# Kernel tuning notes

Measured on AMD Instinct MI355X. Metric: run time of the kernel, lower is better.

## Reference

```python
import jax, jax.numpy as jnp
import numpy as np

B, N, D = 32, 1024, 3
Z_SCALES = jnp.array([2.0, 4.0, 8.0, 16.0, 32.0], dtype=jnp.float32)
Z_DIM = 16.0
BETA = 0.01          # kl_warmup done (epoch >= kl_warmup_epochs), so beta == args.beta
SINK_EPS = 0.1       # entropic regularization for the EMD (Sinkhorn) approximation
SINK_ITERS = 20
BIG = 1e8
NEG = -1e9


def _sqdist(x, y):
    # x: [B,N,D], y: [B,M,D] -> squared euclidean distances [B,N,M]
    xx = jnp.sum(x * x, -1)[:, :, None]
    yy = jnp.sum(y * y, -1)[:, None, :]
    xy = jnp.einsum('bnd,bmd->bnm', x, y)
    return jnp.maximum(xx + yy - 2.0 * xy, 0.0)


def _chamfer(x, xm, y, ym):
    # masked bidirectional chamfer: mean over valid points, mean over batch
    d = _sqdist(x, y)                                             # [B,N,M]
    d_xy = jnp.min(jnp.where(ym[:, None, :], d, BIG), axis=2)     # [B,N]
    d_yx = jnp.min(jnp.where(xm[:, :, None], d, BIG), axis=1)     # [B,M]
    nx = jnp.sum(xm, -1).astype(x.dtype)
    ny = jnp.sum(ym, -1).astype(x.dtype)
    cd = (jnp.sum(jnp.where(xm, d_xy, 0.0), -1) / nx
          + jnp.sum(jnp.where(ym, d_yx, 0.0), -1) / ny)
    return jnp.mean(cd)


def _emd_sinkhorn(x, xm, y, ym):
    # entropic-OT approximation of the masked EMD (log-domain Sinkhorn)
    C = _sqdist(x, y)                                             # [B,N,M]
    C = jnp.where(xm[:, :, None] & ym[:, None, :], C, BIG)
    nx = jnp.sum(xm, -1).astype(x.dtype)                          # [B]
    ny = jnp.sum(ym, -1).astype(x.dtype)
    log_a = jnp.where(xm, -jnp.log(nx)[:, None], NEG)             # [B,N]
    log_b = jnp.where(ym, -jnp.log(ny)[:, None], NEG)             # [B,M]

    @jax.checkpoint
    def step(carry, _):
        f, g = carry
        f = SINK_EPS * (log_a - jax.nn.logsumexp((g[:, None, :] - C) / SINK_EPS, axis=2))
        g = SINK_EPS * (log_b - jax.nn.logsumexp((f[:, :, None] - C) / SINK_EPS, axis=1))
        return (f, g), None

    f0 = jnp.zeros_like(log_a)
    g0 = jnp.zeros_like(log_b)
    (f, g), _ = jax.lax.scan(step, (f0, g0), None, length=SINK_ITERS)
    logP = (f[:, :, None] + g[:, None, :] - C) / SINK_EPS         # transport plan (log)
    emd = jnp.sum(jnp.exp(logP) * C, axis=(1, 2))                 # [B]
    return jnp.mean(emd)


def setup_inputs() -> dict:
    key = jax.random.key(0)
    k1, k2, k3 = jax.random.split(key, 3)
    return {
        'output_set': jax.random.normal(k1, (B, N, D), dtype=jnp.float32),
        'output_mask': jnp.ones((B, N), dtype=bool),
        'target_set': jax.random.normal(k2, (B, N, D), dtype=jnp.float32),
        'target_mask': jnp.ones((B, N), dtype=bool),
        'kls': jax.random.uniform(k3, (B, Z_SCALES.shape[0]), dtype=jnp.float32),
    }


def reference(output_set, output_mask, target_set, target_mask, kls):
    cd = _chamfer(output_set, output_mask, target_set, target_mask)
    emd = _emd_sinkhorn(output_set, output_mask, target_set, target_mask)
    recon_loss = cd + emd
    kl_loss = jnp.mean(jnp.sum(kls, axis=1))
    loss = BETA * kl_loss + recon_loss
    topdown_kl = jnp.mean(kls, axis=0) / (Z_SCALES * Z_DIM)        # [L]
    return loss, kl_loss, recon_loss, topdown_kl
```

## Files before the change

kernel.cpp:

```cpp
#include <hip/hip_runtime.h>
#include <math.h>

#define BB 32
#define NN 1024
#define NEGV (-1e9f)
#define BIGC (1e8f)
#define EPSS 0.1f
#define K2f   14.426950408889634f
#define TWOK2 28.853900817779268f
#define INVK2 0.06931471805599453f
#define SINK_ITERS 20
#define CHUNKS 16
#define NBLK (BB * CHUNKS)
#define BARSTRIDE 32

typedef float f32x2 __attribute__((ext_vector_type(2)));

__device__ __forceinline__ float wave_reduce_sum(float v) {
#pragma unroll
  for (int s = 32; s >= 1; s >>= 1) v += __shfl_xor(v, s, 64);
  return v;
}
__device__ __forceinline__ float wave_reduce_max(float v) {
#pragma unroll
  for (int s = 32; s >= 1; s >>= 1) v = fmaxf(v, __shfl_xor(v, s, 64));
  return v;
}
__device__ __forceinline__ float wave_reduce_min(float v) {
#pragma unroll
  for (int s = 32; s >= 1; s >>= 1) v = fminf(v, __shfl_xor(v, s, 64));
  return v;
}

__device__ __forceinline__ bool getbit(const unsigned* mb, int i) {
  return (mb[i >> 5] >> (i & 31)) & 1u;
}

__device__ __forceinline__ void pot_st2(float* p, float lo, float hi) {
  const unsigned long long pk =
      ((unsigned long long)__float_as_uint(hi) << 32) | __float_as_uint(lo);
  __hip_atomic_store((unsigned long long*)p, pk, __ATOMIC_RELAXED,
                     __HIP_MEMORY_SCOPE_AGENT);
}
__device__ __forceinline__ void pot_ld2(const float* p, float& lo, float& hi) {
  const unsigned long long pk = __hip_atomic_load(
      (const unsigned long long*)p, __ATOMIC_RELAXED, __HIP_MEMORY_SCOPE_AGENT);
  lo = __uint_as_float((unsigned)pk);
  hi = __uint_as_float((unsigned)(pk >> 32));
}
__device__ __forceinline__ float pot_ld(const float* p) {
  return __hip_atomic_load(p, __ATOMIC_RELAXED, __HIP_MEMORY_SCOPE_AGENT);
}

__device__ __forceinline__ void batch_barrier(int* bp, int gen, int tid) {
  __syncthreads();
  if (tid == 0) {
    __hip_atomic_fetch_add(bp, 1, __ATOMIC_RELAXED, __HIP_MEMORY_SCOPE_AGENT);
    const int target = CHUNKS * gen;
    while (__hip_atomic_load(bp, __ATOMIC_RELAXED, __HIP_MEMORY_SCOPE_AGENT) < target)
      __builtin_amdgcn_s_sleep(2);
    (void)__hip_atomic_load(bp, __ATOMIC_ACQUIRE, __HIP_MEMORY_SCOPE_WORKGROUP);
  }
  __syncthreads();
}

template<bool CHAMF>
__device__ __forceinline__ void twopass(
    const float4* rl, const float4* cl, const float* Agl, const unsigned* rmb,
    float elab, int c, int wave, int lane, int tid,
    float* __restrict__ potOut, size_t base,
    float invnb, int b, float* __restrict__ cdPart, float* reds)
{
  float cdacc = 0.0f;
#pragma unroll 1
  for (int grp = 0; grp < 2; ++grp) {
    const int row0 = c * 64 + wave * 8 + grp * 4;

    float xs0[4], xs1[4], xs2[4], xw[4];
    bool rmv[4];
#pragma unroll
    for (int r = 0; r < 4; ++r) {
      const float4 xp = rl[row0 + r];
      xs0[r] = TWOK2 * xp.x; xs1[r] = TWOK2 * xp.y; xs2[r] = TWOK2 * xp.z;
      xw[r] = xp.w;
      rmv[r] = getbit(rmb, row0 + r);
    }

    float u[4][16];
#pragma unroll
    for (int j = 0; j < 16; ++j) {
      const int m = lane + j * 64;
      const float4 yp = cl[m];
      const float aj = Agl[m];
#pragma unroll
      for (int r = 0; r < 4; ++r) {
        float t = fmaf(xs0[r], yp.x, aj);
        t = fmaf(xs1[r], yp.y, t);
        t = fmaf(xs2[r], yp.z, t);
        u[r][j] = t;
      }
    }

    float gm[4];
#pragma unroll
    for (int r = 0; r < 4; ++r) {
      const float a0 = fmaxf(fmaxf(u[r][0], u[r][1]), u[r][2]);
      const float a1 = fmaxf(fmaxf(u[r][3], u[r][4]), u[r][5]);
      const float a2 = fmaxf(fmaxf(u[r][6], u[r][7]), u[r][8]);
      const float a3 = fmaxf(fmaxf(u[r][9], u[r][10]), u[r][11]);
      const float a4 = fmaxf(fmaxf(u[r][12], u[r][13]), u[r][14]);
      const float mr = fmaxf(fmaxf(fmaxf(a0, a1), a2),
                             fmaxf(fmaxf(a3, a4), u[r][15]));
      gm[r] = wave_reduce_max(mr);
    }

    float ss[4] = {0.f, 0.f, 0.f, 0.f};
#pragma unroll
    for (int j = 0; j < 16; ++j) {
#pragma unroll
      for (int r = 0; r < 4; ++r)
        ss[r] += __builtin_amdgcn_exp2f(u[r][j] - gm[r]);
    }
#pragma unroll
    for (int r = 0; r < 4; ++r) ss[r] = wave_reduce_sum(ss[r]);

    float pv[4];
#pragma unroll
    for (int r = 0; r < 4; ++r) {
      const float lse2 = gm[r] + __builtin_amdgcn_logf(ss[r]);
      const float el = rmv[r] ? elab : (EPSS * NEGV);
      pv[r] = el + xw[r] - INVK2 * lse2;
    }
    if (lane == 0) {
      pot_st2(&potOut[base + row0 + 0], pv[0], pv[1]);
      pot_st2(&potOut[base + row0 + 2], pv[2], pv[3]);
      if constexpr (CHAMF) {
#pragma unroll
        for (int r = 0; r < 4; ++r)
          if (rmv[r]) cdacc += fmaxf(fmaf(-INVK2, gm[r], xw[r]), 0.0f);
      }
    }
  }

  if constexpr (CHAMF) {
    if (lane == 0) reds[wave] = cdacc;
    __syncthreads();
    if (tid == 0) {
      float s = 0.f;
#pragma unroll
      for (int w = 0; w < 8; ++w) s += reds[w];
      cdPart[(size_t)b * CHUNKS + c] = s * invnb * (1.0f / BB);
    }
  }
}

__device__ __forceinline__ void onepass(
    const float4* rl, const float4* cl, const float* Agl, const unsigned* rmb,
    float elab, int row0, int lane, float* __restrict__ pot, size_t base,
    float fp[8])
{
  f32x2 xs0[4], xs1[4], xs2[4], sh2[4], acc2[4];
  bool rmv[8];
#pragma unroll
  for (int p = 0; p < 4; ++p) {
    const float4 xa = rl[row0 + 2 * p];
    const float4 xb = rl[row0 + 2 * p + 1];
    rmv[2 * p]     = getbit(rmb, row0 + 2 * p);
    rmv[2 * p + 1] = getbit(rmb, row0 + 2 * p + 1);
    xs0[p] = f32x2{TWOK2 * xa.x, TWOK2 * xb.x};
    xs1[p] = f32x2{TWOK2 * xa.y, TWOK2 * xb.y};
    xs2[p] = f32x2{TWOK2 * xa.z, TWOK2 * xb.z};
    sh2[p] = f32x2{
        rmv[2 * p]     ? (K2f * (elab + xa.w - fp[2 * p]))     : 3.0e38f,
        rmv[2 * p + 1] ? (K2f * (elab + xb.w - fp[2 * p + 1])) : 3.0e38f};
    acc2[p] = f32x2{0.f, 0.f};
  }

#pragma unroll 4
  for (int j = 0; j < 16; ++j) {
    const int m = lane + j * 64;
    const float4 q = cl[m];
    const float aj = Agl[m];
    const f32x2 qx = {q.x, q.x}, qy = {q.y, q.y}, qz = {q.z, q.z};
    const f32x2 aj2 = {aj, aj};
#pragma unroll
    for (int p = 0; p < 4; ++p) {
      f32x2 t = __builtin_elementwise_fma(xs0[p], qx, aj2);
      t = __builtin_elementwise_fma(xs1[p], qy, t);
      t = __builtin_elementwise_fma(xs2[p], qz, t);
      const f32x2 e = t - sh2[p];
      const f32x2 ex = {__builtin_amdgcn_exp2f(e.x), __builtin_amdgcn_exp2f(e.y)};
      acc2[p] += ex;
    }
  }

  float acc[8];
#pragma unroll
  for (int p = 0; p < 4; ++p) { acc[2 * p] = acc2[p].x; acc[2 * p + 1] = acc2[p].y; }
#pragma unroll
  for (int r = 0; r < 8; ++r) acc[r] = wave_reduce_sum(acc[r]);

#pragma unroll
  for (int r = 0; r < 8; ++r) {
    const float l2 = fminf(fmaxf(__builtin_amdgcn_logf(acc[r]), -120.0f), 120.0f);
    fp[r] = rmv[r] ? (fp[r] - INVK2 * l2) : (EPSS * NEGV);
  }
  if (lane == 0) {
#pragma unroll
    for (int r = 0; r < 8; r += 2)
      pot_st2(&pot[base + row0 + r], fp[r], fp[r + 1]);
  }
}

__global__ __launch_bounds__(512, 4) void fused_sink(
    const float* __restrict__ xset, const int* __restrict__ xm,
    const float* __restrict__ yset, const int* __restrict__ ym,
    float* __restrict__ f, float* __restrict__ g,
    float* __restrict__ cd_part, float* __restrict__ emd_part,
    int* __restrict__ bar)
{
  const int gid = blockIdx.x;
  const int b = gid & (BB - 1), c = gid >> 5;
  const int tid = threadIdx.x, wave = tid >> 6, lane = tid & 63;
  const size_t base = (size_t)b * NN;
  int* bp = bar + b * BARSTRIDE;

  __shared__ float4 xl[NN];
  __shared__ float4 yl[NN];
  __shared__ float Ag[NN];
  __shared__ float gvs[NN];
  __shared__ unsigned xmb[NN / 32], ymb[NN / 32];
  __shared__ float cred[16];
  __shared__ float reds[8];
  __shared__ float sscal[4];

  float cntx = 0.f, cnty = 0.f;
  for (int i = tid; i < NN; i += 512) {
    const size_t ix = (base + (size_t)i) * 3;
    const float x0 = xset[ix], x1 = xset[ix + 1], x2 = xset[ix + 2];
    const float y0 = yset[ix], y1 = yset[ix + 1], y2 = yset[ix + 2];
    xl[i] = make_float4(x0, x1, x2, x0 * x0 + x1 * x1 + x2 * x2);
    yl[i] = make_float4(y0, y1, y2, y0 * y0 + y1 * y1 + y2 * y2);
    const int mxv = xm[base + i], myv = ym[base + i];
    cntx += mxv ? 1.0f : 0.0f;
    cnty += myv ? 1.0f : 0.0f;
    const unsigned long long bx = __ballot(mxv != 0);
    const unsigned long long by = __ballot(myv != 0);
    if (lane == 0) {
      const int w0 = i >> 5;
      xmb[w0] = (unsigned)bx; xmb[w0 + 1] = (unsigned)(bx >> 32);
      ymb[w0] = (unsigned)by; ymb[w0 + 1] = (unsigned)(by >> 32);
    }
  }
  cntx = wave_reduce_sum(cntx);
  cnty = wave_reduce_sum(cnty);
  if (lane == 0) { cred[wave] = cntx; cred[8 + wave] = cnty; }
  __syncthreads();
  if (tid == 0) {
    float a = 0.f, cc = 0.f;
#pragma unroll
    for (int i = 0; i < 8; ++i) { a += cred[i]; cc += cred[8 + i]; }
    sscal[0] = -EPSS * logf(a);
    sscal[1] = -EPSS * logf(cc);
    sscal[2] = 1.0f / a;
    sscal[3] = 1.0f / cc;
  }
  __syncthreads();
  const float elax = sscal[0], elay = sscal[1], invx = sscal[2], invy = sscal[3];
  int gen = 0;

  for (int i = tid; i < NN; i += 512)
    Ag[i] = getbit(ymb, i) ? (-K2f * yl[i].w) : -1e30f;
  __syncthreads();
  twopass<true>(xl, yl, Ag, xmb, elax, c, wave, lane, tid, f, base,
                invx, b, cd_part, reds);

  for (int i = tid; i < NN; i += 512)
    gvs[i] = getbit(xmb, i) ? xl[i].w : BIGC;
  __syncthreads();
  {
    float acc = 0.0f;
#pragma unroll 1
    for (int rr = 0; rr < 8; ++rr) {
      const int row = c * 64 + wave * 8 + rr;
      const float4 yp = yl[row];
      const float ys0 = -2.f * yp.x, ys1 = -2.f * yp.y, ys2 = -2.f * yp.z;
      float dmin = BIGC;
#pragma unroll
      for (int j = 0; j < 16; ++j) {
        const int m = lane + j * 64;
        const float4 xq = xl[m];
        float d = fmaf(ys0, xq.x, gvs[m]);
        d = fmaf(ys1, xq.y, d);
        d = fmaf(ys2, xq.z, d);
        dmin = fminf(dmin, d);
      }
      dmin = wave_reduce_min(dmin);
      if (lane == 0 && getbit(ymb, row)) acc += fmaxf(yp.w + dmin, 0.0f);
    }
    __syncthreads();
    if (lane == 0) reds[wave] = acc;
    __syncthreads();
    if (tid == 0) {
      float s = 0.f;
#pragma unroll
      for (int w = 0; w < 8; ++w) s += reds[w];
      cd_part[BB * CHUNKS + (size_t)b * CHUNKS + c] = s * invy * (1.0f / BB);
    }
  }

  batch_barrier(bp, ++gen, tid);

  {
    const int i2 = tid << 1;
    float f0, f1;
    pot_ld2(&f[base + i2], f0, f1);
    Ag[i2]     = getbit(xmb, i2)     ? fmaf(K2f, f0, -K2f * xl[i2].w)     : -1e30f;
    Ag[i2 + 1] = getbit(xmb, i2 + 1) ? fmaf(K2f, f1, -K2f * xl[i2 + 1].w) : -1e30f;
  }
  __syncthreads();
  twopass<false>(yl, xl, Ag, ymb, elay, c, wave, lane, tid, g, base,
                 0.f, b, nullptr, reds);

  float myf[8], myg[8];
  __syncthreads();
  {
    const int row0w = c * 64 + wave * 8;
#pragma unroll
    for (int r = 0; r < 8; r += 2) {
      pot_ld2(&f[base + row0w + r], myf[r], myf[r + 1]);
      pot_ld2(&g[base + row0w + r], myg[r], myg[r + 1]);
    }
  }

  batch_barrier(bp, ++gen, tid);

  const int row0w = c * 64 + wave * 8;
  for (int it = 1; it < SINK_ITERS; ++it) {
    {
      const int i2 = tid << 1;
      float g0, g1;
      pot_ld2(&g[base + i2], g0, g1);
      Ag[i2]     = getbit(ymb, i2)     ? fmaf(K2f, g0, -K2f * yl[i2].w)     : -1e30f;
      Ag[i2 + 1] = getbit(ymb, i2 + 1) ? fmaf(K2f, g1, -K2f * yl[i2 + 1].w) : -1e30f;
    }
    __syncthreads();
    onepass(xl, yl, Ag, xmb, elax, row0w, lane, f, base, myf);
    batch_barrier(bp, ++gen, tid);

    {
      const int i2 = tid << 1;
      float f0, f1;
      pot_ld2(&f[base + i2], f0, f1);
      Ag[i2]     = getbit(xmb, i2)     ? fmaf(K2f, f0, -K2f * xl[i2].w)     : -1e30f;
      Ag[i2 + 1] = getbit(xmb, i2 + 1) ? fmaf(K2f, f1, -K2f * xl[i2 + 1].w) : -1e30f;
    }
    __syncthreads();
    onepass(yl, xl, Ag, ymb, elay, row0w, lane, g, base, myg);
    batch_barrier(bp, ++gen, tid);
  }

  {
    const int i2 = tid << 1;
    float g0, g1;
    pot_ld2(&g[base + i2], g0, g1);
    gvs[i2] = g0; gvs[i2 + 1] = g1;
    Ag[i2]     = getbit(ymb, i2)     ? fmaf(K2f, g0, -K2f * yl[i2].w)     : -1e30f;
    Ag[i2 + 1] = getbit(ymb, i2 + 1) ? fmaf(K2f, g1, -K2f * yl[i2 + 1].w) : -1e30f;
  }
  __syncthreads();
  {
    float acc = 0.0f;
#pragma unroll 1
    for (int rr = 0; rr < 8; ++rr) {
      const int row = c * 64 + wave * 8 + rr;
      const float4 xp = xl[row];
      const float fv = pot_ld(&f[base + row]);
      const float rc = fmaf(K2f, fv, -K2f * xp.w);
      const float xs0 = TWOK2 * xp.x, xs1 = TWOK2 * xp.y, xs2 = TWOK2 * xp.z;
      const bool rv = getbit(xmb, row);
#pragma unroll
      for (int j = 0; j < 16; ++j) {
        const int m = lane + j * 64;
        const float4 yp = yl[m];
        const float a = rv ? (Ag[m] + rc) : -1e30f;
        float t = fmaf(xs0, yp.x, a);
        t = fmaf(xs1, yp.y, t);
        t = fmaf(xs2, yp.z, t);
        float C = fmaf(t, -INVK2, fv + gvs[m]);
        C = fmaxf(C, 0.0f);
        acc = fmaf(__builtin_amdgcn_exp2f(t), C, acc);
      }
    }
    acc = wave_reduce_sum(acc);
    __syncthreads();
    if (lane == 0) reds[wave] = acc;
    __syncthreads();
    if (tid == 0) {
      float s = 0.f;
#pragma unroll
      for (int w = 0; w < 8; ++w) s += reds[w];
      emd_part[(size_t)b * CHUNKS + c] = s * (1.0f / BB);
    }
  }
}

__global__ __launch_bounds__(1024) void prep_kernel(
    const float* __restrict__ xset, const int* __restrict__ xm,
    const float* __restrict__ yset, const int* __restrict__ ym,
    float4* __restrict__ xpack, float4* __restrict__ ypack,
    float* __restrict__ elax, float* __restrict__ elay,
    float* __restrict__ invx, float* __restrict__ invy)
{
  const int b = blockIdx.x;
  const int n = threadIdx.x;
  const size_t idx = (size_t)b * NN + n;

  const float x0 = xset[idx * 3 + 0], x1 = xset[idx * 3 + 1], x2 = xset[idx * 3 + 2];
  const float y0 = yset[idx * 3 + 0], y1 = yset[idx * 3 + 1], y2 = yset[idx * 3 + 2];
  xpack[idx] = make_float4(x0, x1, x2, x0 * x0 + x1 * x1 + x2 * x2);
  ypack[idx] = make_float4(y0, y1, y2, y0 * y0 + y1 * y1 + y2 * y2);

  float cx = wave_reduce_sum(xm[idx] ? 1.0f : 0.0f);
  float cy = wave_reduce_sum(ym[idx] ? 1.0f : 0.0f);

  __shared__ float sx[16], sy[16];
  const int wave = n >> 6, lane = n & 63;
  if (lane == 0) { sx[wave] = cx; sy[wave] = cy; }
  __syncthreads();
  if (n == 0) {
    float a = 0.0f, c = 0.0f;
#pragma unroll
    for (int i = 0; i < 16; ++i) { a += sx[i]; c += sy[i]; }
    elax[b] = -EPSS * logf(a);
    elay[b] = -EPSS * logf(c);
    invx[b] = 1.0f / a;
    invy[b] = 1.0f / c;
  }
}

template<bool FIRST, bool CHAMF>
__global__ __launch_bounds__(512) void sink_step(
    const float4* __restrict__ rowpk, const float4* __restrict__ redpk,
    const int* __restrict__ rowmask, const int* __restrict__ redmask,
    const float* __restrict__ pot_in, float* __restrict__ pot_out,
    const float* __restrict__ ela,
    const float* __restrict__ invn,
    float* __restrict__ cd_part)
{
  const int b = blockIdx.y, chunk = blockIdx.x, tid = threadIdx.x;
  const int wave = tid >> 6, lane = tid & 63;
  const size_t base = (size_t)b * NN;

  __shared__ float4 ypk[NN];
  __shared__ float Aj[NN];
  __shared__ float reds[8];

  for (int i = tid; i < NN; i += 512) {
    const float4 yp = redpk[base + i];
    ypk[i] = yp;
    float a;
    if constexpr (FIRST)
      a = redmask[base + i] ? (-K2f * yp.w) : -1e30f;
    else
      a = redmask[base + i] ? fmaf(K2f, pot_in[base + i], -K2f * yp.w) : -1e30f;
    Aj[i] = a;
  }
  __syncthreads();

  const float elab = ela[b];
  float cdacc = 0.0f;

#pragma unroll 1
  for (int grp = 0; grp < 2; ++grp) {
    const int row0 = chunk * 64 + wave * 8 + grp * 4;

    float xs0[4], xs1[4], xs2[4], xw[4];
    int rmv[4];
#pragma unroll
    for (int r = 0; r < 4; ++r) {
      const float4 xp = rowpk[base + row0 + r];
      xs0[r] = TWOK2 * xp.x; xs1[r] = TWOK2 * xp.y; xs2[r] = TWOK2 * xp.z;
      xw[r] = xp.w;
      rmv[r] = rowmask[base + row0 + r];
    }

    float u[4][16];
#pragma unroll
    for (int j = 0; j < 16; ++j) {
      const int m = lane + j * 64;
      const float4 yp = ypk[m];
      const float aj = Aj[m];
#pragma unroll
      for (int r = 0; r < 4; ++r) {
        float t = fmaf(xs0[r], yp.x, aj);
        t = fmaf(xs1[r], yp.y, t);
        t = fmaf(xs2[r], yp.z, t);
        u[r][j] = t;
      }
    }

    float gm[4];
#pragma unroll
    for (int r = 0; r < 4; ++r) {
      const float a0 = fmaxf(fmaxf(u[r][0], u[r][1]), u[r][2]);
      const float a1 = fmaxf(fmaxf(u[r][3], u[r][4]), u[r][5]);
      const float a2 = fmaxf(fmaxf(u[r][6], u[r][7]), u[r][8]);
      const float a3 = fmaxf(fmaxf(u[r][9], u[r][10]), u[r][11]);
      const float a4 = fmaxf(fmaxf(u[r][12], u[r][13]), u[r][14]);
      const float mr = fmaxf(fmaxf(fmaxf(a0, a1), a2),
                             fmaxf(fmaxf(a3, a4), u[r][15]));
      gm[r] = wave_reduce_max(mr);
    }

    float ss[4] = {0.f, 0.f, 0.f, 0.f};
#pragma unroll
    for (int j = 0; j < 16; ++j) {
#pragma unroll
      for (int r = 0; r < 4; ++r)
        ss[r] += __builtin_amdgcn_exp2f(u[r][j] - gm[r]);
    }
#pragma unroll
    for (int r = 0; r < 4; ++r) ss[r] = wave_reduce_sum(ss[r]);

    if (lane == 0) {
#pragma unroll
      for (int r = 0; r < 4; ++r) {
        const float lse2 = gm[r] + __builtin_amdgcn_logf(ss[r]);
        const float el = rmv[r] ? elab : (EPSS * NEGV);
        pot_out[base + row0 + r] = el + xw[r] - INVK2 * lse2;
        if constexpr (CHAMF) {
          if (rmv[r])
            cdacc += fmaxf(fmaf(-INVK2, gm[r], xw[r]), 0.0f);
        }
      }
    }
  }

  if constexpr (CHAMF) {
    if (lane == 0) reds[wave] = cdacc;
    __syncthreads();
    if (tid == 0) {
      float s = 0.f;
#pragma unroll
      for (int w = 0; w < 8; ++w) s += reds[w];
      cd_part[(size_t)b * CHUNKS + chunk] = s * invn[b] * (1.0f / BB);
    }
  }
}

__global__ __launch_bounds__(512) void sink_fast(
    const float4* __restrict__ rowpk, const float4* __restrict__ redpk,
    const int* __restrict__ rowmask, const int* __restrict__ redmask,
    const float* __restrict__ pot_in, float* __restrict__ fpot,
    const float* __restrict__ ela)
{
  const int b = blockIdx.y, chunk = blockIdx.x, tid = threadIdx.x;
  const int wave = tid >> 6, lane = tid & 63;
  const size_t base = (size_t)b * NN;

  __shared__ float4 colq[NN];

  for (int i = tid; i < NN; i += 512) {
    const float4 yp = redpk[base + i];
    const float aj = redmask[base + i]
        ? fmaf(K2f, pot_in[base + i], -K2f * yp.w) : -1e30f;
    colq[i] = make_float4(yp.x, yp.y, yp.z, aj);
  }
  __syncthreads();

  const float elab = ela[b];
  const int row0 = chunk * 64 + wave * 8;

  float xs0[8], xs1[8], xs2[8], sh[8], acc[8], fp[8];
  int rmv[8];
#pragma unroll
  for (int r = 0; r < 8; ++r) {
    const float4 xp = rowpk[base + row0 + r];
    rmv[r] = rowmask[base + row0 + r];
    fp[r] = fpot[base + row0 + r];
    xs0[r] = TWOK2 * xp.x; xs1[r] = TWOK2 * xp.y; xs2[r] = TWOK2 * xp.z;
    sh[r] = rmv[r] ? (K2f * (elab + xp.w - fp[r])) : 3.0e38f;
    acc[r] = 0.0f;
  }

#pragma unroll 4
  for (int j = 0; j < 16; ++j) {
    const float4 q = colq[lane + j * 64];
#pragma unroll
    for (int r = 0; r < 8; ++r) {
      float t = fmaf(xs0[r], q.x, q.w);
      t = fmaf(xs1[r], q.y, t);
      t = fmaf(xs2[r], q.z, t);
      acc[r] += __builtin_amdgcn_exp2f(t - sh[r]);
    }
  }

#pragma unroll
  for (int r = 0; r < 8; ++r) acc[r] = wave_reduce_sum(acc[r]);

  if (lane == 0) {
#pragma unroll
    for (int r = 0; r < 8; ++r) {
      const float l2 = fminf(fmaxf(__builtin_amdgcn_logf(acc[r]), -120.0f), 120.0f);
      fpot[base + row0 + r] = rmv[r] ? (fp[r] - INVK2 * l2) : (EPSS * NEGV);
    }
  }
}

__global__ __launch_bounds__(512) void chamfer_dir(
    const float4* __restrict__ rowpk, const float4* __restrict__ redpk,
    const int* __restrict__ rowmask, const int* __restrict__ redmask,
    const float* __restrict__ invn, float* __restrict__ part)
{
  const int b = blockIdx.y, chunk = blockIdx.x, tid = threadIdx.x;
  const int wave = tid >> 6, lane = tid & 63;
  const size_t base = (size_t)b * NN;

  __shared__ float4 xw4[NN];
  for (int i = tid; i < NN; i += 512) {
    float4 xp = redpk[base + i];
    xp.w = redmask[base + i] ? xp.w : BIGC;
    xw4[i] = xp;
  }
  __syncthreads();

  float acc = 0.0f;
#pragma unroll 1
  for (int rr = 0; rr < 8; ++rr) {
    const int row = chunk * 64 + wave * 8 + rr;
    const float4 yp = rowpk[base + row];
    const float ys0 = -2.f * yp.x, ys1 = -2.f * yp.y, ys2 = -2.f * yp.z;
    float dmin = BIGC;
#pragma unroll
    for (int j = 0; j < 16; ++j) {
      const float4 xq = xw4[lane + j * 64];
      float d = fmaf(ys0, xq.x, xq.w);
      d = fmaf(ys1, xq.y, d);
      d = fmaf(ys2, xq.z, d);
      dmin = fminf(dmin, d);
    }
    dmin = wave_reduce_min(dmin);
    if (lane == 0 && rowmask[base + row]) acc += fmaxf(yp.w + dmin, 0.0f);
  }

  __shared__ float reds[8];
  if (lane == 0) reds[wave] = acc;
  __syncthreads();
  if (tid == 0) {
    float s = 0.f;
#pragma unroll
    for (int w = 0; w < 8; ++w) s += reds[w];
    part[(size_t)b * CHUNKS + chunk] = s * invn[b] * (1.0f / BB);
  }
}

__global__ __launch_bounds__(512) void emd_kernel(
    const float4* __restrict__ rowpk, const float4* __restrict__ redpk,
    const int* __restrict__ rowmask, const int* __restrict__ redmask,
    const float* __restrict__ frow, const float* __restrict__ gred,
    float* __restrict__ part)
{
  const int b = blockIdx.y, chunk = blockIdx.x, tid = threadIdx.x;
  const int wave = tid >> 6, lane = tid & 63;
  const size_t base = (size_t)b * NN;

  __shared__ float4 ypk[NN];
  __shared__ float Ag[NN];
  __shared__ float gv[NN];
  for (int i = tid; i < NN; i += 512) {
    const float4 yp = redpk[base + i];
    ypk[i] = yp;
    const float gg = gred[base + i];
    gv[i] = gg;
    Ag[i] = redmask[base + i] ? fmaf(K2f, gg, -K2f * yp.w) : -1e30f;
  }
  __syncthreads();

  float acc = 0.0f;
#pragma unroll 1
  for (int rr = 0; rr < 8; ++rr) {
    const int row = chunk * 64 + wave * 8 + rr;
    const float4 xp = rowpk[base + row];
    const float fv = frow[base + row];
    const float rc = fmaf(K2f, fv, -K2f * xp.w);
    const float xs0 = TWOK2 * xp.x, xs1 = TWOK2 * xp.y, xs2 = TWOK2 * xp.z;
    const bool rv = rowmask[base + row] != 0;
#pragma unroll
    for (int j = 0; j < 16; ++j) {
      const int m = lane + j * 64;
      const float4 yp = ypk[m];
      const float a = rv ? (Ag[m] + rc) : -1e30f;
      float t = fmaf(xs0, yp.x, a);
      t = fmaf(xs1, yp.y, t);
      t = fmaf(xs2, yp.z, t);
      float C = fmaf(t, -INVK2, fv + gv[m]);
      C = fmaxf(C, 0.0f);
      acc = fmaf(__builtin_amdgcn_exp2f(t), C, acc);
    }
  }

  acc = wave_reduce_sum(acc);
  __shared__ float reds[8];
  if (lane == 0) reds[wave] = acc;
  __syncthreads();
  if (tid == 0) {
    float s = 0.f;
#pragma unroll
    for (int w = 0; w < 8; ++w) s += reds[w];
    part[(size_t)b * CHUNKS + chunk] = s * (1.0f / BB);
  }
}

__global__ __launch_bounds__(256) void final_kernel(
    const float* __restrict__ cd_part, const float* __restrict__ emd_part,
    const float* __restrict__ kls, float* __restrict__ out)
{
  const int tid = threadIdx.x, wave = tid >> 6, lane = tid & 63;
  __shared__ float sh[12];
  float s1 = 0.f, s2 = 0.f, s3 = 0.f;
  for (int i = tid; i < 2 * BB * CHUNKS; i += 256) s1 += cd_part[i];
  for (int i = tid; i < BB * CHUNKS; i += 256) s2 += emd_part[i];
  for (int i = tid; i < BB * 5; i += 256) s3 += kls[i];
  s1 = wave_reduce_sum(s1); s2 = wave_reduce_sum(s2); s3 = wave_reduce_sum(s3);
  if (lane == 0) { sh[wave] = s1; sh[4 + wave] = s2; sh[8 + wave] = s3; }
  __syncthreads();
  if (tid == 0) {
    const float cd = sh[0] + sh[1] + sh[2] + sh[3];
    const float emd = sh[4] + sh[5] + sh[6] + sh[7];
    const float kl = (sh[8] + sh[9] + sh[10] + sh[11]) / (float)BB;
    out[0] = 0.01f * kl + (cd + emd);
    out[1] = kl;
    out[2] = cd + emd;
  }
  if (tid < 5) {
    float cs = 0.f;
    for (int b2 = 0; b2 < BB; ++b2) cs += kls[b2 * 5 + tid];
    const float zs[5] = {2.f, 4.f, 8.f, 16.f, 32.f};
    out[3 + tid] = (cs / (float)BB) / (zs[tid] * 16.f);
  }
}

extern "C" void kernel_launch(void* const* d_in, const int* in_sizes, int n_in,
                              void* d_out, int out_size, void* d_ws, size_t ws_size,
                              hipStream_t stream)
{
  const float* xset = (const float*)d_in[0];
  const int*   xm   = (const int*)d_in[1];
  const float* yset = (const float*)d_in[2];
  const int*   ym   = (const int*)d_in[3];
  const float* kls  = (const float*)d_in[4];

  float* ws = (float*)d_ws;
  float*  f    = ws;
  float*  g    = f + BB * NN;
  float*  cd   = g + BB * NN;
  float*  emdp = cd + 2 * BB * CHUNKS;
  float*  elax = emdp + BB * CHUNKS;
  float*  elay = elax + BB;
  float*  invx = elay + BB;
  float*  invy = invx + BB;
  int*    bar  = (int*)(invy + BB);
  float4* xp4  = (float4*)(ws + 68256);
  float4* yp4  = xp4 + BB * NN;

  hipMemsetAsync(bar, 0, BB * BARSTRIDE * sizeof(int), stream);

  void* args[] = {(void*)&xset, (void*)&xm, (void*)&yset, (void*)&ym,
                  (void*)&f, (void*)&g, (void*)&cd, (void*)&emdp, (void*)&bar};
  hipError_t cerr = hipLaunchCooperativeKernel(
      reinterpret_cast<void*>(fused_sink), dim3(NBLK), dim3(512), args, 0, stream);

  if (cerr != hipSuccess) {
    prep_kernel<<<dim3(BB), 1024, 0, stream>>>(xset, xm, yset, ym,
                                               xp4, yp4, elax, elay, invx, invy);
    const dim3 sg(CHUNKS, BB);
    sink_step<true, true><<<sg, 512, 0, stream>>>(xp4, yp4, xm, ym, nullptr, f,
                                                  elax, invx, cd);
    chamfer_dir<<<sg, 512, 0, stream>>>(yp4, xp4, ym, xm, invy, cd + BB * CHUNKS);
    sink_step<false, false><<<sg, 512, 0, stream>>>(yp4, xp4, ym, xm, f, g,
                                                    elay, nullptr, nullptr);
    for (int it = 1; it < SINK_ITERS; ++it) {
      sink_fast<<<sg, 512, 0, stream>>>(xp4, yp4, xm, ym, g, f, elax);
      sink_fast<<<sg, 512, 0, stream>>>(yp4, xp4, ym, xm, f, g, elay);
    }
    emd_kernel<<<sg, 512, 0, stream>>>(xp4, yp4, xm, ym, f, g, emdp);
  }

  final_kernel<<<1, 256, 0, stream>>>(cd, emdp, kls, (float*)d_out);
}
```

Baseline: 382.9 us.

## Interleave two batch streams per block to hide inter-block barrier latency

After: 480.5 us. +25.5%, slower.

```diff
diff --git a/kernel.cpp b/kernel.cpp
--- a/kernel.cpp
+++ b/kernel.cpp
@@ -11,7 +11,7 @@
 #define INVK2 0.06931471805599453f
 #define SINK_ITERS 20
 #define CHUNKS 16
-#define NBLK (BB * CHUNKS)
+#define NBLK 256
 #define BARSTRIDE 32
 
 typedef float f32x2 __attribute__((ext_vector_type(2)));
@@ -52,13 +52,16 @@
   return __hip_atomic_load(p, __ATOMIC_RELAXED, __HIP_MEMORY_SCOPE_AGENT);
 }
 
-__device__ __forceinline__ void batch_barrier(int* bp, int gen, int tid) {
-  __syncthreads();
+__device__ __forceinline__ void bar_arrive(int* bp, int tid) {
+  __syncthreads();
+  if (tid == 0)
+    __hip_atomic_fetch_add(bp, 1, __ATOMIC_RELAXED, __HIP_MEMORY_SCOPE_AGENT);
+}
+__device__ __forceinline__ void bar_wait(int* bp, int gen, int tid) {
   if (tid == 0) {
-    __hip_atomic_fetch_add(bp, 1, __ATOMIC_RELAXED, __HIP_MEMORY_SCOPE_AGENT);
     const int target = CHUNKS * gen;
     while (__hip_atomic_load(bp, __ATOMIC_RELAXED, __HIP_MEMORY_SCOPE_AGENT) < target)
-      __builtin_amdgcn_s_sleep(2);
+      __builtin_amdgcn_s_sleep(1);
     (void)__hip_atomic_load(bp, __ATOMIC_ACQUIRE, __HIP_MEMORY_SCOPE_WORKGROUP);
   }
   __syncthreads();
@@ -212,28 +215,13 @@
   }
 }
 
-__global__ __launch_bounds__(512, 4) void fused_sink(
+__device__ __forceinline__ void stage_stream(
     const float* __restrict__ xset, const int* __restrict__ xm,
     const float* __restrict__ yset, const int* __restrict__ ym,
-    float* __restrict__ f, float* __restrict__ g,
-    float* __restrict__ cd_part, float* __restrict__ emd_part,
-    int* __restrict__ bar)
-{
-  const int gid = blockIdx.x;
-  const int b = gid & (BB - 1), c = gid >> 5;
-  const int tid = threadIdx.x, wave = tid >> 6, lane = tid & 63;
-  const size_t base = (size_t)b * NN;
-  int* bp = bar + b * BARSTRIDE;
-
-  __shared__ float4 xl[NN];
-  __shared__ float4 yl[NN];
-  __shared__ float Ag[NN];
-  __shared__ float gvs[NN];
-  __shared__ unsigned xmb[NN / 32], ymb[NN / 32];
-  __shared__ float cred[16];
-  __shared__ float reds[8];
-  __shared__ float sscal[4];
-
+    size_t base, int tid, int lane, int wave,
+    float4* xl, float4* yl, unsigned* xmb, unsigned* ymb,
+    float* cred, float* sscal4)
+{
   float cntx = 0.f, cnty = 0.f;
   for (int i = tid; i < NN; i += 512) {
     const size_t ix = (base + (size_t)i) * 3;
@@ -260,106 +248,88 @@
     float a = 0.f, cc = 0.f;
 #pragma unroll
     for (int i = 0; i < 8; ++i) { a += cred[i]; cc += cred[8 + i]; }
-    sscal[0] = -EPSS * logf(a);
-    sscal[1] = -EPSS * logf(cc);
-    sscal[2] = 1.0f / a;
-    sscal[3] = 1.0f / cc;
-  }
-  __syncthreads();
-  const float elax = sscal[0], elay = sscal[1], invx = sscal[2], invy = sscal[3];
-  int gen = 0;
-
+    sscal4[0] = -EPSS * logf(a);
+    sscal4[1] = -EPSS * logf(cc);
+    sscal4[2] = 1.0f / a;
+    sscal4[3] = 1.0f / cc;
+  }
+  __syncthreads();
+}
+
+__device__ __forceinline__ void build_ag_first(
+    const float4* yl, const unsigned* ymb, float* Ag, int tid)
+{
   for (int i = tid; i < NN; i += 512)
     Ag[i] = getbit(ymb, i) ? (-K2f * yl[i].w) : -1e30f;
   __syncthreads();
-  twopass<true>(xl, yl, Ag, xmb, elax, c, wave, lane, tid, f, base,
-                invx, b, cd_part, reds);
-
+}
+__device__ __forceinline__ void build_ag_pot(
+    const float4* pl, const unsigned* pmb, const float* pot, size_t base,
+    float* Ag, int tid)
+{
+  const int i2 = tid << 1;
+  float p0, p1;
+  pot_ld2(&pot[base + i2], p0, p1);
+  Ag[i2]     = getbit(pmb, i2)     ? fmaf(K2f, p0, -K2f * pl[i2].w)     : -1e30f;
+  Ag[i2 + 1] = getbit(pmb, i2 + 1) ? fmaf(K2f, p1, -K2f * pl[i2 + 1].w) : -1e30f;
+  __syncthreads();
+}
+
+__device__ __forceinline__ void chamfer_yx(
+    const float4* xl, const float4* yl, const unsigned* xmb, const unsigned* ymb,
+    float* gvs, float* reds, int c, int wave, int lane, int tid,
+    float invy, int b, float* __restrict__ cd_part)
+{
   for (int i = tid; i < NN; i += 512)
     gvs[i] = getbit(xmb, i) ? xl[i].w : BIGC;
   __syncthreads();
-  {
-    float acc = 0.0f;
+  float acc = 0.0f;
 #pragma unroll 1
-    for (int rr = 0; rr < 8; ++rr) {
-      const int row = c * 64 + wave * 8 + rr;
-      const float4 yp = yl[row];
-      const float ys0 = -2.f * yp.x, ys1 = -2.f * yp.y, ys2 = -2.f * yp.z;
-      float dmin = BIGC;
-#pragma unroll
-      for (int j = 0; j < 16; ++j) {
-        const int m = lane + j * 64;
-        const float4 xq = xl[m];
-        float d = fmaf(ys0, xq.x, gvs[m]);
-        d = fmaf(ys1, xq.y, d);
-        d = fmaf(ys2, xq.z, d);
-        dmin = fminf(dmin, d);
-      }
-      dmin = wave_reduce_min(dmin);
-      if (lane == 0 && getbit(ymb, row)) acc += fmaxf(yp.w + dmin, 0.0f);
-    }
-    __syncthreads();
-    if (lane == 0) reds[wave] = acc;
-    __syncthreads();
-    if (tid == 0) {
-      float s = 0.f;
-#pragma unroll
-      for (int w = 0; w < 8; ++w) s += reds[w];
-      cd_part[BB * CHUNKS + (size_t)b * CHUNKS + c] = s * invy * (1.0f / BB);
-    }
-  }
-
-  batch_barrier(bp, ++gen, tid);
-
-  {
-    const int i2 = tid << 1;
-    float f0, f1;
-    pot_ld2(&f[base + i2], f0, f1);
-    Ag[i2]     = getbit(xmb, i2)     ? fmaf(K2f, f0, -K2f * xl[i2].w)     : -1e30f;
-    Ag[i2 + 1] = getbit(xmb, i2 + 1) ? fmaf(K2f, f1, -K2f * xl[i2 + 1].w) : -1e30f;
-  }
-  __syncthreads();
-  twopass<false>(yl, xl, Ag, ymb, elay, c, wave, lane, tid, g, base,
-                 0.f, b, nullptr, reds);
-
-  float myf[8], myg[8];
-  __syncthreads();
-  {
-    const int row0w = c * 64 + wave * 8;
-#pragma unroll
-    for (int r = 0; r < 8; r += 2) {
-      pot_ld2(&f[base + row0w + r], myf[r], myf[r + 1]);
-      pot_ld2(&g[base + row0w + r], myg[r], myg[r + 1]);
-    }
-  }
-
-  batch_barrier(bp, ++gen, tid);
-
-  const int row0w = c * 64 + wave * 8;
-  for (int it = 1; it < SINK_ITERS; ++it) {
-    {
-      const int i2 = tid << 1;
-      float g0, g1;
-      pot_ld2(&g[base + i2], g0, g1);
-      Ag[i2]     = getbit(ymb, i2)     ? fmaf(K2f, g0, -K2f * yl[i2].w)     : -1e30f;
-      Ag[i2 + 1] = getbit(ymb, i2 + 1) ? fmaf(K2f, g1, -K2f * yl[i2 + 1].w) : -1e30f;
-    }
-    __syncthreads();
-    onepass(xl, yl, Ag, xmb, elax, row0w, lane, f, base, myf);
-    batch_barrier(bp, ++gen, tid);
-
-    {
-      const int i2 = tid << 1;
-      float f0, f1;
-      pot_ld2(&f[base + i2], f0, f1);
-      Ag[i2]     = getbit(xmb, i2)     ? fmaf(K2f, f0, -K2f * xl[i2].w)     : -1e30f;
-      Ag[i2 + 1] = getbit(xmb, i2 + 1) ? fmaf(K2f, f1, -K2f * xl[i2 + 1].w) : -1e30f;
-    }
-    __syncthreads();
-    onepass(yl, xl, Ag, ymb, elay, row0w, lane, g, base, myg);
-    batch_barrier(bp, ++gen, tid);
-  }
-
+  for (int rr = 0; rr < 8; ++rr) {
+    const int row = c * 64 + wave * 8 + rr;
+    const float4 yp = yl[row];
+    const float ys0 = -2.f * yp.x, ys1 = -2.f * yp.y, ys2 = -2.f * yp.z;
+    float dmin = BIGC;
+#pragma unroll
+    for (int j = 0; j < 16; ++j) {
+      const int m = lane + j * 64;
+      const float4 xq = xl[m];
+      float d = fmaf(ys0, xq.x, gvs[m]);
+      d = fmaf(ys1, xq.y, d);
+      d = fmaf(ys2, xq.z, d);
+      dmin = fminf(dmin, d);
+    }
+    dmin = wave_reduce_min(dmin);
+    if (lane == 0 && getbit(ymb, row)) acc += fmaxf(yp.w + dmin, 0.0f);
+  }
+  __syncthreads();
+  if (lane == 0) reds[wave] = acc;
+  __syncthreads();
+  if (tid == 0) {
+    float s = 0.f;
+#pragma unroll
+    for (int w = 0; w < 8; ++w) s += reds[w];
+    cd_part[BB * CHUNKS + (size_t)b * CHUNKS + c] = s * invy * (1.0f / BB);
+  }
+}
+
+__device__ __forceinline__ void pull_rows(
+    const float* f, const float* g, size_t base, int row0w,
+    float myf[8], float myg[8])
+{
+#pragma unroll
+  for (int r = 0; r < 8; r += 2) {
+    pot_ld2(&f[base + row0w + r], myf[r], myf[r + 1]);
+    pot_ld2(&g[base + row0w + r], myg[r], myg[r + 1]);
+  }
+}
+
+__device__ __forceinline__ void emd_eval(
+    const float4* xl, const float4* yl, const unsigned* xmb, const unsigned* ymb,
+    const float* f, const float* g, size_t base,
+    float* Ag, float* gvs, float* reds,
+    int c, int wave, int lane, int tid, int b, float* __restrict__ emd_part)
+{
   {
     const int i2 = tid << 1;
     float g0, g1;
@@ -369,40 +339,130 @@
     Ag[i2 + 1] = getbit(ymb, i2 + 1) ? fmaf(K2f, g1, -K2f * yl[i2 + 1].w) : -1e30f;
   }
   __syncthreads();
-  {
-    float acc = 0.0f;
+  float acc = 0.0f;
 #pragma unroll 1
-    for (int rr = 0; rr < 8; ++rr) {
-      const int row = c * 64 + wave * 8 + rr;
-      const float4 xp = xl[row];
-      const float fv = pot_ld(&f[base + row]);
-      const float rc = fmaf(K2f, fv, -K2f * xp.w);
-      const float xs0 = TWOK2 * xp.x, xs1 = TWOK2 * xp.y, xs2 = TWOK2 * xp.z;
-      const bool rv = getbit(xmb, row);
-#pragma unroll
-      for (int j = 0; j < 16; ++j) {
-        const int m = lane + j * 64;
-        const float4 yp = yl[m];
-        const float a = rv ? (Ag[m] + rc) : -1e30f;
-        float t = fmaf(xs0, yp.x, a);
-        t = fmaf(xs1, yp.y, t);
-        t = fmaf(xs2, yp.z, t);
-        float C = fmaf(t, -INVK2, fv + gvs[m]);
-        C = fmaxf(C, 0.0f);
-        acc = fmaf(__builtin_amdgcn_exp2f(t), C, acc);
-      }
-    }
-    acc = wave_reduce_sum(acc);
-    __syncthreads();
-    if (lane == 0) reds[wave] = acc;
-    __syncthreads();
-    if (tid == 0) {
-      float s = 0.f;
-#pragma unroll
-      for (int w = 0; w < 8; ++w) s += reds[w];
-      emd_part[(size_t)b * CHUNKS + c] = s * (1.0f / BB);
-    }
-  }
+  for (int rr = 0; rr < 8; ++rr) {
+    const int row = c * 64 + wave * 8 + rr;
+    const float4 xp = xl[row];
+    const float fv = pot_ld(&f[base + row]);
+    const float rc = fmaf(K2f, fv, -K2f * xp.w);
+    const float xs0 = TWOK2 * xp.x, xs1 = TWOK2 * xp.y, xs2 = TWOK2 * xp.z;
+    const bool rv = getbit(xmb, row);
+#pragma unroll
+    for (int j = 0; j < 16; ++j) {
+      const int m = lane + j * 64;
+      const float4 yp = yl[m];
+      const float a = rv ? (Ag[m] + rc) : -1e30f;
+      float t = fmaf(xs0, yp.x, a);
+      t = fmaf(xs1, yp.y, t);
+      t = fmaf(xs2, yp.z, t);
+      float C = fmaf(t, -INVK2, fv + gvs[m]);
+      C = fmaxf(C, 0.0f);
+      acc = fmaf(__builtin_amdgcn_exp2f(t), C, acc);
+    }
+  }
+  acc = wave_reduce_sum(acc);
+  __syncthreads();
+  if (lane == 0) reds[wave] = acc;
+  __syncthreads();
+  if (tid == 0) {
+    float s = 0.f;
+#pragma unroll
+    for (int w = 0; w < 8; ++w) s += reds[w];
+    emd_part[(size_t)b * CHUNKS + c] = s * (1.0f / BB);
+  }
+}
+
+__global__ __launch_bounds__(512, 2) void fused_sink(
+    const float* __restrict__ xset, const int* __restrict__ xm,
+    const float* __restrict__ yset, const int* __restrict__ ym,
+    float* __restrict__ f, float* __restrict__ g,
+    float* __restrict__ cd_part, float* __restrict__ emd_part,
+    int* __restrict__ bar)
+{
+  const int i = blockIdx.x;
+  const int bA = i & (BB - 1), cA = i >> 5;
+  const int bB = (i + 16) & (BB - 1), cB = (i >> 5) + 8;
+  const int tid = threadIdx.x, wave = tid >> 6, lane = tid & 63;
+  const size_t baseA = (size_t)bA * NN, baseB = (size_t)bB * NN;
+  int* bpA = bar + bA * BARSTRIDE;
+  int* bpB = bar + bB * BARSTRIDE;
+
+  __shared__ float4 xlA[NN], ylA[NN];
+  __shared__ float4 xlB[NN], ylB[NN];
+  __shared__ float Ag[NN];
+  __shared__ float gvs[NN];
+  __shared__ unsigned xmbA[NN / 32], ymbA[NN / 32], xmbB[NN / 32], ymbB[NN / 32];
+  __shared__ float cred[16];
+  __shared__ float reds[8];
+  __shared__ float sscal[8];
+
+  stage_stream(xset, xm, yset, ym, baseA, tid, lane, wave,
+               xlA, ylA, xmbA, ymbA, cred, sscal + 0);
+  stage_stream(xset, xm, yset, ym, baseB, tid, lane, wave,
+               xlB, ylB, xmbB, ymbB, cred, sscal + 4);
+  const float elaxA = sscal[0], elayA = sscal[1], invxA = sscal[2], invyA = sscal[3];
+  const float elaxB = sscal[4], elayB = sscal[5], invxB = sscal[6], invyB = sscal[7];
+
+  build_ag_first(ylA, ymbA, Ag, tid);
+  twopass<true>(xlA, ylA, Ag, xmbA, elaxA, cA, wave, lane, tid, f, baseA,
+                invxA, bA, cd_part, reds);
+  chamfer_yx(xlA, ylA, xmbA, ymbA, gvs, reds, cA, wave, lane, tid, invyA, bA, cd_part);
+  bar_arrive(bpA, tid);
+
+  build_ag_first(ylB, ymbB, Ag, tid);
+  twopass<true>(xlB, ylB, Ag, xmbB, elaxB, cB, wave, lane, tid, f, baseB,
+                invxB, bB, cd_part, reds);
+  chamfer_yx(xlB, ylB, xmbB, ymbB, gvs, reds, cB, wave, lane, tid, invyB, bB, cd_part);
+  bar_arrive(bpB, tid);
+
+  float myfA[8], mygA[8], myfB[8], mygB[8];
+  const int row0A = cA * 64 + wave * 8, row0B = cB * 64 + wave * 8;
+
+  bar_wait(bpA, 1, tid);
+  build_ag_pot(xlA, xmbA, f, baseA, Ag, tid);
+  twopass<false>(ylA, xlA, Ag, ymbA, elayA, cA, wave, lane, tid, g, baseA,
+                 0.f, bA, nullptr, reds);
+  __syncthreads();
+  pull_rows(f, g, baseA, row0A, myfA, mygA);
+  bar_arrive(bpA, tid);
+
+  bar_wait(bpB, 1, tid);
+  build_ag_pot(xlB, xmbB, f, baseB, Ag, tid);
+  twopass<false>(ylB, xlB, Ag, ymbB, elayB, cB, wave, lane, tid, g, baseB,
+                 0.f, bB, nullptr, reds);
+  __syncthreads();
+  pull_rows(f, g, baseB, row0B, myfB, mygB);
+  bar_arrive(bpB, tid);
+
+  for (int it = 1; it < SINK_ITERS; ++it) {
+    bar_wait(bpA, 2 * it, tid);
+    build_ag_pot(ylA, ymbA, g, baseA, Ag, tid);
+    onepass(xlA, ylA, Ag, xmbA, elaxA, row0A, lane, f, baseA, myfA);
+    bar_arrive(bpA, tid);
+
+    bar_wait(bpB, 2 * it, tid);
+    build_ag_pot(ylB, ymbB, g, baseB, Ag, tid);
+    onepass(xlB, ylB, Ag, xmbB, elaxB, row0B, lane, f, baseB, myfB);
+    bar_arrive(bpB, tid);
+
+    bar_wait(bpA, 2 * it + 1, tid);
+    build_ag_pot(xlA, xmbA, f, baseA, Ag, tid);
+    onepass(ylA, xlA, Ag, ymbA, elayA, row0A, lane, g, baseA, mygA);
+    bar_arrive(bpA, tid);
+
+    bar_wait(bpB, 2 * it + 1, tid);
+    build_ag_pot(xlB, xmbB, f, baseB, Ag, tid);
+    onepass(ylB, xlB, Ag, ymbB, elayB, row0B, lane, g, baseB, mygB);
+    bar_arrive(bpB, tid);
+  }
+
+  bar_wait(bpA, 2 * SINK_ITERS, tid);
+  emd_eval(xlA, ylA, xmbA, ymbA, f, g, baseA, Ag, gvs, reds,
+           cA, wave, lane, tid, bA, emd_part);
+  bar_wait(bpB, 2 * SINK_ITERS, tid);
+  emd_eval(xlB, ylB, xmbB, ymbB, f, g, baseB, Ag, gvs, reds,
+           cB, wave, lane, tid, bB, emd_part);
 }
 
 __global__ __launch_bounds__(1024) void prep_kernel(
```

## Replace per-batch barriers with per-chunk flags and stream potentials into Sinkhorn pass

Applied to the files above, without the earlier changes.

After: 652.5 us. 1.7x slower.

```diff
diff --git a/kernel.cpp b/kernel.cpp
--- a/kernel.cpp
+++ b/kernel.cpp
@@ -51,15 +51,17 @@
 __device__ __forceinline__ float pot_ld(const float* p) {
   return __hip_atomic_load(p, __ATOMIC_RELAXED, __HIP_MEMORY_SCOPE_AGENT);
 }
-
-__device__ __forceinline__ void batch_barrier(int* bp, int gen, int tid) {
-  __syncthreads();
-  if (tid == 0) {
-    __hip_atomic_fetch_add(bp, 1, __ATOMIC_RELAXED, __HIP_MEMORY_SCOPE_AGENT);
-    const int target = CHUNKS * gen;
-    while (__hip_atomic_load(bp, __ATOMIC_RELAXED, __HIP_MEMORY_SCOPE_AGENT) < target)
-      __builtin_amdgcn_s_sleep(2);
-    (void)__hip_atomic_load(bp, __ATOMIC_ACQUIRE, __HIP_MEMORY_SCOPE_WORKGROUP);
+__device__ __forceinline__ int flag_ld(const int* p) {
+  return __hip_atomic_load(p, __ATOMIC_RELAXED, __HIP_MEMORY_SCOPE_AGENT);
+}
+
+__device__ __forceinline__ void flag_bump(int* fl) {
+  __hip_atomic_fetch_add(fl, 1, __ATOMIC_RELAXED, __HIP_MEMORY_SCOPE_AGENT);
+}
+
+__device__ __forceinline__ void wait_all16(const int* flags, int gen, int tid) {
+  if (tid < 16) {
+    while (flag_ld(&flags[tid]) < gen) __builtin_amdgcn_s_sleep(2);
   }
   __syncthreads();
 }
@@ -69,7 +71,7 @@
     const float4* rl, const float4* cl, const float* Agl, const unsigned* rmb,
     float elab, int c, int wave, int lane, int tid,
     float* __restrict__ potOut, size_t base,
-    float invnb, int b, float* __restrict__ cdPart, float* reds)
+    float invnb, int b, float* __restrict__ cdPart, float* reds, float myp[8])
 {
   float cdacc = 0.0f;
 #pragma unroll 1
@@ -130,6 +132,7 @@
       const float lse2 = gm[r] + __builtin_amdgcn_logf(ss[r]);
       const float el = rmv[r] ? elab : (EPSS * NEGV);
       pv[r] = el + xw[r] - INVK2 * lse2;
+      myp[grp * 4 + r] = pv[r];
     }
     if (lane == 0) {
       pot_st2(&potOut[base + row0 + 0], pv[0], pv[1]);
@@ -154,11 +157,15 @@
   }
 }
 
-__device__ __forceinline__ void onepass(
-    const float4* rl, const float4* cl, const float* Agl, const unsigned* rmb,
-    float elab, int row0, int lane, float* __restrict__ pot, size_t base,
-    float fp[8])
-{
+__device__ __forceinline__ void onepass_stream(
+    const float4* rl, const float4* cl, const unsigned* cmb,
+    const float* __restrict__ potIn, const int* __restrict__ cflags, int gen,
+    float elab, int row0, int lane, float* __restrict__ potOut, size_t base,
+    float fp[8], const unsigned* rmb)
+{
+  while (flag_ld(&cflags[0]) < gen) __builtin_amdgcn_s_sleep(1);
+  float pv = pot_ld(&potIn[base + lane]);
+
   f32x2 xs0[4], xs1[4], xs2[4], sh2[4], acc2[4];
   bool rmv[8];
 #pragma unroll
@@ -178,9 +185,14 @@
 
 #pragma unroll 4
   for (int j = 0; j < 16; ++j) {
+    float pvn = 0.0f;
+    if (j < 15) {
+      while (flag_ld(&cflags[j + 1]) < gen) __builtin_amdgcn_s_sleep(1);
+      pvn = pot_ld(&potIn[base + (j + 1) * 64 + lane]);
+    }
     const int m = lane + j * 64;
     const float4 q = cl[m];
-    const float aj = Agl[m];
+    const float aj = getbit(cmb, m) ? fmaf(K2f, pv, -K2f * q.w) : -1e30f;
     const f32x2 qx = {q.x, q.x}, qy = {q.y, q.y}, qz = {q.z, q.z};
     const f32x2 aj2 = {aj, aj};
 #pragma unroll
@@ -192,6 +204,7 @@
       const f32x2 ex = {__builtin_amdgcn_exp2f(e.x), __builtin_amdgcn_exp2f(e.y)};
       acc2[p] += ex;
     }
+    pv = pvn;
   }
 
   float acc[8];
@@ -208,7 +221,7 @@
   if (lane == 0) {
 #pragma unroll
     for (int r = 0; r < 8; r += 2)
-      pot_st2(&pot[base + row0 + r], fp[r], fp[r + 1]);
+      pot_st2(&potOut[base + row0 + r], fp[r], fp[r + 1]);
   }
 }
 
@@ -223,7 +236,8 @@
   const int b = gid & (BB - 1), c = gid >> 5;
   const int tid = threadIdx.x, wave = tid >> 6, lane = tid & 63;
   const size_t base = (size_t)b * NN;
-  int* bp = bar + b * BARSTRIDE;
+  int* fflags = bar + b * BARSTRIDE;
+  int* gflags = fflags + 16;
 
   __shared__ float4 xl[NN];
   __shared__ float4 yl[NN];
@@ -267,13 +281,16 @@
   }
   __syncthreads();
   const float elax = sscal[0], elay = sscal[1], invx = sscal[2], invy = sscal[3];
-  int gen = 0;
+
+  float myf[8], myg[8];
+  const int row0w = c * 64 + wave * 8;
 
   for (int i = tid; i < NN; i += 512)
     Ag[i] = getbit(ymb, i) ? (-K2f * yl[i].w) : -1e30f;
   __syncthreads();
   twopass<true>(xl, yl, Ag, xmb, elax, c, wave, lane, tid, f, base,
-                invx, b, cd_part, reds);
+                invx, b, cd_part, reds, myf);
+  if (tid == 0) flag_bump(&fflags[c]);
 
   for (int i = tid; i < NN; i += 512)
     gvs[i] = getbit(xmb, i) ? xl[i].w : BIGC;
@@ -309,8 +326,7 @@
     }
   }
 
-  batch_barrier(bp, ++gen, tid);
-
+  wait_all16(fflags, 1, tid);
   {
     const int i2 = tid << 1;
     float f0, f1;
@@ -320,46 +336,22 @@
   }
   __syncthreads();
   twopass<false>(yl, xl, Ag, ymb, elay, c, wave, lane, tid, g, base,
-                 0.f, b, nullptr, reds);
-
-  float myf[8], myg[8];
-  __syncthreads();
-  {
-    const int row0w = c * 64 + wave * 8;
-#pragma unroll
-    for (int r = 0; r < 8; r += 2) {
-      pot_ld2(&f[base + row0w + r], myf[r], myf[r + 1]);
-      pot_ld2(&g[base + row0w + r], myg[r], myg[r + 1]);
-    }
-  }
-
-  batch_barrier(bp, ++gen, tid);
-
-  const int row0w = c * 64 + wave * 8;
+                 0.f, b, nullptr, reds, myg);
+  __syncthreads();
+  if (tid == 0) flag_bump(&gflags[c]);
+
   for (int it = 1; it < SINK_ITERS; ++it) {
-    {
-      const int i2 = tid << 1;
-      float g0, g1;
-      pot_ld2(&g[base + i2], g0, g1);
-      Ag[i2]     = getbit(ymb, i2)     ? fmaf(K2f, g0, -K2f * yl[i2].w)     : -1e30f;
-      Ag[i2 + 1] = getbit(ymb, i2 + 1) ? fmaf(K2f, g1, -K2f * yl[i2 + 1].w) : -1e30f;
-    }
+    onepass_stream(xl, yl, ymb, g, gflags, it, elax, row0w, lane, f, base,
+                   myf, xmb);
     __syncthreads();
-    onepass(xl, yl, Ag, xmb, elax, row0w, lane, f, base, myf);
-    batch_barrier(bp, ++gen, tid);
-
-    {
-      const int i2 = tid << 1;
-      float f0, f1;
-      pot_ld2(&f[base + i2], f0, f1);
-      Ag[i2]     = getbit(xmb, i2)     ? fmaf(K2f, f0, -K2f * xl[i2].w)     : -1e30f;
-      Ag[i2 + 1] = getbit(xmb, i2 + 1) ? fmaf(K2f, f1, -K2f * xl[i2 + 1].w) : -1e30f;
-    }
+    if (tid == 0) flag_bump(&fflags[c]);
+    onepass_stream(yl, xl, xmb, f, fflags, it + 1, elay, row0w, lane, g, base,
+                   myg, ymb);
     __syncthreads();
-    onepass(yl, xl, Ag, ymb, elay, row0w, lane, g, base, myg);
-    batch_barrier(bp, ++gen, tid);
-  }
-
+    if (tid == 0) flag_bump(&gflags[c]);
+  }
+
+  wait_all16(gflags, SINK_ITERS, tid);
   {
     const int i2 = tid << 1;
     float g0, g1;
@@ -373,9 +365,9 @@
     float acc = 0.0f;
 #pragma unroll 1
     for (int rr = 0; rr < 8; ++rr) {
-      const int row = c * 64 + wave * 8 + rr;
+      const int row = row0w + rr;
       const float4 xp = xl[row];
-      const float fv = pot_ld(&f[base + row]);
+      const float fv = myf[rr];
       const float rc = fmaf(K2f, fv, -K2f * xp.w);
       const float xs0 = TWOK2 * xp.x, xs1 = TWOK2 * xp.y, xs2 = TWOK2 * xp.z;
       const bool rv = getbit(xmb, row);
```

## Replace per-batch workgroup barriers with per-wave arrival flags for f and g

Applied to the files above, without the earlier changes.

New measurement: 644.2 us. 68.2% more time.

```diff
diff --git a/kernel.cpp b/kernel.cpp
--- a/kernel.cpp
+++ b/kernel.cpp
@@ -12,7 +12,8 @@
 #define SINK_ITERS 20
 #define CHUNKS 16
 #define NBLK (BB * CHUNKS)
-#define BARSTRIDE 32
+#define BARSTRIDE 64
+#define ARRV (8 * CHUNKS)
 
 typedef float f32x2 __attribute__((ext_vector_type(2)));
 
@@ -52,14 +53,17 @@
   return __hip_atomic_load(p, __ATOMIC_RELAXED, __HIP_MEMORY_SCOPE_AGENT);
 }
 
-__device__ __forceinline__ void batch_barrier(int* bp, int gen, int tid) {
-  __syncthreads();
+__device__ __forceinline__ void wave_publish(int* fl, int lane) {
+  asm volatile("s_waitcnt vmcnt(0)" ::: "memory");
+  if (lane == 0)
+    __hip_atomic_fetch_add(fl, 1, __ATOMIC_RELAXED, __HIP_MEMORY_SCOPE_AGENT);
+}
+
+__device__ __forceinline__ void wg_wait(const int* fl, int gen, int tid) {
   if (tid == 0) {
-    __hip_atomic_fetch_add(bp, 1, __ATOMIC_RELAXED, __HIP_MEMORY_SCOPE_AGENT);
-    const int target = CHUNKS * gen;
-    while (__hip_atomic_load(bp, __ATOMIC_RELAXED, __HIP_MEMORY_SCOPE_AGENT) < target)
-      __builtin_amdgcn_s_sleep(2);
-    (void)__hip_atomic_load(bp, __ATOMIC_ACQUIRE, __HIP_MEMORY_SCOPE_WORKGROUP);
+    const int target = ARRV * gen;
+    while (__hip_atomic_load(fl, __ATOMIC_RELAXED, __HIP_MEMORY_SCOPE_AGENT) < target)
+      __builtin_amdgcn_s_sleep(1);
   }
   __syncthreads();
 }
@@ -69,7 +73,7 @@
     const float4* rl, const float4* cl, const float* Agl, const unsigned* rmb,
     float elab, int c, int wave, int lane, int tid,
     float* __restrict__ potOut, size_t base,
-    float invnb, int b, float* __restrict__ cdPart, float* reds)
+    float invnb, int b, float* __restrict__ cdPart, float* reds, float myp[8])
 {
   float cdacc = 0.0f;
 #pragma unroll 1
@@ -130,6 +134,7 @@
       const float lse2 = gm[r] + __builtin_amdgcn_logf(ss[r]);
       const float el = rmv[r] ? elab : (EPSS * NEGV);
       pv[r] = el + xw[r] - INVK2 * lse2;
+      myp[grp * 4 + r] = pv[r];
     }
     if (lane == 0) {
       pot_st2(&potOut[base + row0 + 0], pv[0], pv[1]);
@@ -223,7 +228,8 @@
   const int b = gid & (BB - 1), c = gid >> 5;
   const int tid = threadIdx.x, wave = tid >> 6, lane = tid & 63;
   const size_t base = (size_t)b * NN;
-  int* bp = bar + b * BARSTRIDE;
+  int* fflag = bar + b * BARSTRIDE;
+  int* gflag = fflag + 32;
 
   __shared__ float4 xl[NN];
   __shared__ float4 yl[NN];
@@ -267,14 +273,16 @@
   }
   __syncthreads();
   const float elax = sscal[0], elay = sscal[1], invx = sscal[2], invy = sscal[3];
-  int gen = 0;
+
+  float myf[8], myg[8];
+  const int row0w = c * 64 + wave * 8;
 
   for (int i = tid; i < NN; i += 512)
     Ag[i] = getbit(ymb, i) ? (-K2f * yl[i].w) : -1e30f;
   __syncthreads();
   twopass<true>(xl, yl, Ag, xmb, elax, c, wave, lane, tid, f, base,
-                invx, b, cd_part, reds);
-
+                invx, b, cd_part, reds, myf);
+  wave_publish(fflag, lane);
   for (int i = tid; i < NN; i += 512)
     gvs[i] = getbit(xmb, i) ? xl[i].w : BIGC;
   __syncthreads();
@@ -309,8 +317,7 @@
     }
   }
 
-  batch_barrier(bp, ++gen, tid);
-
+  wg_wait(fflag, 1, tid);
   {
     const int i2 = tid << 1;
     float f0, f1;
@@ -320,23 +327,11 @@
   }
   __syncthreads();
   twopass<false>(yl, xl, Ag, ymb, elay, c, wave, lane, tid, g, base,
-                 0.f, b, nullptr, reds);
-
-  float myf[8], myg[8];
-  __syncthreads();
-  {
-    const int row0w = c * 64 + wave * 8;
-#pragma unroll
-    for (int r = 0; r < 8; r += 2) {
-      pot_ld2(&f[base + row0w + r], myf[r], myf[r + 1]);
-      pot_ld2(&g[base + row0w + r], myg[r], myg[r + 1]);
-    }
-  }
-
-  batch_barrier(bp, ++gen, tid);
-
-  const int row0w = c * 64 + wave * 8;
+                 0.f, b, nullptr, reds, myg);
+  wave_publish(gflag, lane);
+
   for (int it = 1; it < SINK_ITERS; ++it) {
+    wg_wait(gflag, it, tid);
     {
       const int i2 = tid << 1;
       float g0, g1;
@@ -346,8 +341,9 @@
     }
     __syncthreads();
     onepass(xl, yl, Ag, xmb, elax, row0w, lane, f, base, myf);
-    batch_barrier(bp, ++gen, tid);
-
+    wave_publish(fflag, lane);
+
+    wg_wait(fflag, it + 1, tid);
     {
       const int i2 = tid << 1;
       float f0, f1;
@@ -357,9 +353,10 @@
     }
     __syncthreads();
     onepass(yl, xl, Ag, ymb, elay, row0w, lane, g, base, myg);
-    batch_barrier(bp, ++gen, tid);
-  }
-
+    wave_publish(gflag, lane);
+  }
+
+  wg_wait(gflag, SINK_ITERS, tid);
   {
     const int i2 = tid << 1;
     float g0, g1;
@@ -373,9 +370,9 @@
     float acc = 0.0f;
 #pragma unroll 1
     for (int rr = 0; rr < 8; ++rr) {
-      const int row = c * 64 + wave * 8 + rr;
+      const int row = row0w + rr;
       const float4 xp = xl[row];
-      const float fv = pot_ld(&f[base + row]);
+      const float fv = myf[rr];
       const float rc = fmaf(K2f, fv, -K2f * xp.w);
       const float xs0 = TWOK2 * xp.x, xs1 = TWOK2 * xp.y, xs2 = TWOK2 * xp.z;
       const bool rv = getbit(xmb, row);
@@ -761,7 +758,7 @@
   float*  invx = elay + BB;
   float*  invy = invx + BB;
   int*    bar  = (int*)(invy + BB);
-  float4* xp4  = (float4*)(ws + 68256);
+  float4* xp4  = (float4*)(ws + 69248);
   float4* yp4  = xp4 + BB * NN;
 
   hipMemsetAsync(bar, 0, BB * BARSTRIDE * sizeof(int), stream);
```
